# Optimization experiments

Hardware: AMD Instinct MI355X
Metric: run time of the kernel (lower is better)

## Reference

```python
import jax, jax.numpy as jnp
import numpy as np

B, S, D = 32, 4096, 64
EPS_DIV = 1e-8
EPS_LN = 1e-5  # torch LayerNorm default


def setup_inputs() -> dict:
    key = jax.random.key(0)
    k1, k2, k3 = jax.random.split(key, 3)
    C = jax.random.normal(k1, (B, S, D), dtype=jnp.float32)
    V = jax.random.normal(k2, (B, S, D), dtype=jnp.float32)
    W = jax.random.normal(k3, (B, S, D), dtype=jnp.float32)
    time_mod = jnp.ones((1, 1, D), dtype=jnp.float32) * 0.5  # matches init: ones * 0.5
    ln_gamma = jnp.ones((D,), dtype=jnp.float32)
    ln_beta = jnp.zeros((D,), dtype=jnp.float32)
    return {"C": C, "V": V, "W": W, "time_mod": time_mod,
            "ln_gamma": ln_gamma, "ln_beta": ln_beta}


def reference(C, V, W, time_mod, ln_gamma, ln_beta):
    # Precompute elementwise quantities once (fused, no per-step kernels)
    decay = jax.nn.sigmoid(W * time_mod)        # [B,S,D]
    eC = jnp.exp(C)                             # [B,S,D]

    # scan over sequence axis; move S to the front for lax.scan
    xs = (jnp.swapaxes(decay, 0, 1),            # [S,B,D]
          jnp.swapaxes(eC, 0, 1),
          jnp.swapaxes(V, 0, 1))

    a0 = jnp.zeros((C.shape[0], 1), dtype=C.dtype)
    b0 = jnp.zeros((C.shape[0], C.shape[2]), dtype=C.dtype)

    def step(carry, x):
        a, b = carry
        d, ec, v = x                            # each [B,D]
        a = jnp.mean(d, axis=1, keepdims=True) * a + jnp.sum(ec, axis=1, keepdims=True)
        b = d * b + ec * v
        return (a, b), b / (a + EPS_DIV)

    _, ys = jax.lax.scan(step, (a0, b0), xs)    # ys: [S,B,D]
    result = jnp.swapaxes(ys, 0, 1)             # [B,S,D]

    # LayerNorm over last dim
    mu = jnp.mean(result, axis=-1, keepdims=True)
    var = jnp.var(result, axis=-1, keepdims=True)
    normed = (result - mu) * jax.lax.rsqrt(var + EPS_LN)
    return normed * ln_gamma + ln_beta
```

## Files before the change

kernel.cpp:

```cpp
#include <hip/hip_runtime.h>
#include <hip/hip_fp16.h>

constexpr int B = 32, S = 4096, D = 64;
constexpr float EPS_DIV = 1e-8f;
constexpr float EPS_LN  = 1e-5f;

constexpr int NCG = 512;
constexpr int LG  = S / NCG;
constexpr int CPL = NCG / 64;
constexpr int BPB = NCG / 16;

struct alignas(16) H2x4 { __half2 a, b, c, d; };

typedef float        f4v __attribute__((ext_vector_type(4)));
typedef unsigned int u2v __attribute__((ext_vector_type(2)));

__device__ __forceinline__ void nt_store_f4(float4 v, float4* p) {
    f4v t = {v.x, v.y, v.z, v.w};
    __builtin_nontemporal_store(t, (f4v*)p);
}

__device__ __forceinline__ float sigmoid_f(float x) {
    return __builtin_amdgcn_rcpf(1.f + __expf(-x));
}

__global__ __launch_bounds__(256, 4) void k1h(
    const float4* __restrict__ C4, const float4* __restrict__ V4,
    const float4* __restrict__ W4, const float* __restrict__ TM,
    float2* __restrict__ MQstep,
    float*  __restrict__ Mc, float* __restrict__ Qc,
    H2x4*   __restrict__ POt,
    H2x4*   __restrict__ dgev)
{
    __shared__ float sp[64][17];
    __shared__ float so[64][17];

    const int t = threadIdx.x;
    const int g = t >> 4;
    const int r = t & 15;
    const int G = blockIdx.x * 16 + g;
    const int b = G >> 9;
    const int c = G & (NCG - 1);
    const int c0 = (blockIdx.x & (BPB - 1)) * 16;
    const int s0 = c * LG;
    const size_t base = (size_t)(b * S + s0) * 16 + r;
    const float4 tm = reinterpret_cast<const float4*>(TM)[r];

    float psd[LG], pse[LG];
    float4 P = {1.f, 1.f, 1.f, 1.f}, O = {0.f, 0.f, 0.f, 0.f};
#pragma unroll
    for (int i = 0; i < LG; ++i) {
        const size_t idx = base + (size_t)i * 16;
        const float4 w = W4[idx], cc = C4[idx], v = V4[idx];
        float4 dg, ec;
        dg.x = sigmoid_f(w.x * tm.x); dg.y = sigmoid_f(w.y * tm.y);
        dg.z = sigmoid_f(w.z * tm.z); dg.w = sigmoid_f(w.w * tm.w);
        ec.x = __expf(cc.x); ec.y = __expf(cc.y);
        ec.z = __expf(cc.z); ec.w = __expf(cc.w);
        psd[i] = (dg.x + dg.y) + (dg.z + dg.w);
        pse[i] = (ec.x + ec.y) + (ec.z + ec.w);
        H2x4 hq;
        hq.a = __floats2half2_rn(dg.x, ec.x * v.x);
        hq.b = __floats2half2_rn(dg.y, ec.y * v.y);
        hq.c = __floats2half2_rn(dg.z, ec.z * v.z);
        hq.d = __floats2half2_rn(dg.w, ec.w * v.w);
        dgev[idx] = hq;
        const float2 f0 = __half22float2(hq.a);
        const float2 f1 = __half22float2(hq.b);
        const float2 f2 = __half22float2(hq.c);
        const float2 f3 = __half22float2(hq.d);
        P.x *= f0.x; P.y *= f1.x; P.z *= f2.x; P.w *= f3.x;
        O.x = fmaf(f0.x, O.x, f0.y);
        O.y = fmaf(f1.x, O.y, f1.y);
        O.z = fmaf(f2.x, O.z, f2.y);
        O.w = fmaf(f3.x, O.w, f3.y);
    }

#pragma unroll
    for (int m = 1; m < 16; m <<= 1) {
#pragma unroll
        for (int i = 0; i < LG; ++i) {
            psd[i] += __shfl_xor(psd[i], m, 64);
            pse[i] += __shfl_xor(pse[i], m, 64);
        }
    }
    float M = 1.f, Q = 0.f;
#pragma unroll
    for (int i = 0; i < LG; ++i) {
        const float mm = psd[i] * (1.f / 64.f);
        M *= mm;
        Q  = fmaf(mm, Q, pse[i]);
    }
    if (r == 0) {
#pragma unroll
        for (int i = 0; i < LG; ++i)
            MQstep[b * S + s0 + i] = make_float2(psd[i] * (1.f / 64.f), pse[i]);
        Mc[G] = M; Qc[G] = Q;
    }

    sp[4*r+0][g] = P.x; sp[4*r+1][g] = P.y; sp[4*r+2][g] = P.z; sp[4*r+3][g] = P.w;
    so[4*r+0][g] = O.x; so[4*r+1][g] = O.y; so[4*r+2][g] = O.z; so[4*r+3][g] = O.w;
    __syncthreads();
    const int d  = t >> 2;
    const int cq = t & 3;
    H2x4 po;
    po.a = __floats2half2_rn(sp[d][cq*4+0], so[d][cq*4+0]);
    po.b = __floats2half2_rn(sp[d][cq*4+1], so[d][cq*4+1]);
    po.c = __floats2half2_rn(sp[d][cq*4+2], so[d][cq*4+2]);
    po.d = __floats2half2_rn(sp[d][cq*4+3], so[d][cq*4+3]);
    POt[(size_t)(b * D + d) * (NCG / 4) + (c0 >> 2) + cq] = po;
}

__global__ __launch_bounds__(256) void k2(
    const float*  __restrict__ Mc,  const float*  __restrict__ Qc,
    const H2x4*   __restrict__ POt,
    float4* __restrict__ aIn4,
    H2x4*   __restrict__ bInH)
{
    const int wq   = threadIdx.x >> 6;
    const int lane = threadIdx.x & 63;

    if (blockIdx.x < 512) {
        const int W = blockIdx.x * 4 + wq;
        const int b = W >> 6, d = W & 63;
        const size_t row4 = (size_t)(b * D + d) * (NCG / 4);
        const H2x4 A = POt[row4 + lane*2], Bq = POt[row4 + lane*2 + 1];
        float pj[CPL], oj[CPL];
        {
            float2 f;
            f = __half22float2(A.a);  pj[0] = f.x; oj[0] = f.y;
            f = __half22float2(A.b);  pj[1] = f.x; oj[1] = f.y;
            f = __half22float2(A.c);  pj[2] = f.x; oj[2] = f.y;
            f = __half22float2(A.d);  pj[3] = f.x; oj[3] = f.y;
            f = __half22float2(Bq.a); pj[4] = f.x; oj[4] = f.y;
            f = __half22float2(Bq.b); pj[5] = f.x; oj[5] = f.y;
            f = __half22float2(Bq.c); pj[6] = f.x; oj[6] = f.y;
            f = __half22float2(Bq.d); pj[7] = f.x; oj[7] = f.y;
        }
        float p = 1.f, o = 0.f;
#pragma unroll
        for (int j = 0; j < CPL; ++j) { o = fmaf(pj[j], o, oj[j]); p = pj[j] * p; }
#pragma unroll
        for (int s = 1; s < 64; s <<= 1) {
            const float pp = __shfl_up(p, s, 64);
            const float oo = __shfl_up(o, s, 64);
            if (lane >= s) { o = fmaf(p, oo, o); p = p * pp; }
        }
        float oe = __shfl_up(o, 1, 64);
        if (lane == 0) oe = 0.f;
        float bv = oe, ob[CPL];
#pragma unroll
        for (int j = 0; j < CPL; ++j) { ob[j] = bv; bv = fmaf(pj[j], bv, oj[j]); }
        H2x4 w;
        w.a = __floats2half2_rn(ob[0], ob[1]);
        w.b = __floats2half2_rn(ob[2], ob[3]);
        w.c = __floats2half2_rn(ob[4], ob[5]);
        w.d = __floats2half2_rn(ob[6], ob[7]);
        bInH[(size_t)(b * D + d) * (NCG / 8) + lane] = w;
    } else {
        const int v = (blockIdx.x - 512) * 4 + wq;
        if (v >= B) return;
        const float4* Mc4 = reinterpret_cast<const float4*>(Mc) + v * (NCG / 4);
        const float4* Qc4 = reinterpret_cast<const float4*>(Qc) + v * (NCG / 4);
        const float4 mA = Mc4[lane*2], mB = Mc4[lane*2 + 1];
        const float4 qA = Qc4[lane*2], qB = Qc4[lane*2 + 1];
        float mj[CPL] = {mA.x, mA.y, mA.z, mA.w, mB.x, mB.y, mB.z, mB.w};
        float qj[CPL] = {qA.x, qA.y, qA.z, qA.w, qB.x, qB.y, qB.z, qB.w};
        float m = 1.f, q = 0.f;
#pragma unroll
        for (int j = 0; j < CPL; ++j) { q = fmaf(mj[j], q, qj[j]); m = mj[j] * m; }
#pragma unroll
        for (int s = 1; s < 64; s <<= 1) {
            const float mm = __shfl_up(m, s, 64);
            const float qq = __shfl_up(q, s, 64);
            if (lane >= s) { q = fmaf(m, qq, q); m = m * mm; }
        }
        float qe = __shfl_up(q, 1, 64);
        if (lane == 0) qe = 0.f;
        float a = qe, ab[CPL];
#pragma unroll
        for (int j = 0; j < CPL; ++j) { ab[j] = a; a = fmaf(mj[j], a, qj[j]); }
        aIn4[v * (NCG / 4) + lane*2]     = make_float4(ab[0], ab[1], ab[2], ab[3]);
        aIn4[v * (NCG / 4) + lane*2 + 1] = make_float4(ab[4], ab[5], ab[6], ab[7]);
    }
}

__global__ __launch_bounds__(256, 4) void k3h(
    const H2x4* __restrict__ dgev,
    const float* __restrict__ Gam, const float* __restrict__ Bet,
    const float2* __restrict__ MQstep,
    const float* __restrict__ aIn, const __half* __restrict__ bInH,
    float4* __restrict__ out4)
{
    __shared__ float sb[64][17];

    const int t = threadIdx.x;
    const int b  = blockIdx.x >> 5;
    const int c0 = (blockIdx.x & (BPB - 1)) * 16;
    {
        const int d = t >> 2, cq = t & 3;
        const u2v raw = *reinterpret_cast<const u2v*>(
            bInH + (size_t)(b * D + d) * NCG + c0 + cq * 4);
        union { unsigned int u; __half2 h; } c0u, c1u;
        c0u.u = raw.x; c1u.u = raw.y;
        const float2 f0 = __half22float2(c0u.h);
        const float2 f1 = __half22float2(c1u.h);
        sb[d][cq*4+0] = f0.x; sb[d][cq*4+1] = f0.y;
        sb[d][cq*4+2] = f1.x; sb[d][cq*4+3] = f1.y;
    }
    __syncthreads();

    const int g = t >> 4;
    const int r = t & 15;
    const int c = c0 + g;
    const int s0 = c * LG;
    const size_t base = (size_t)(b * S + s0) * 16 + r;
    const float4 g4 = reinterpret_cast<const float4*>(Gam)[r];
    const float4 b4 = reinterpret_cast<const float4*>(Bet)[r];

    float a = aIn[b * NCG + c];
    float4 bv = make_float4(sb[4*r+0][g], sb[4*r+1][g],
                            sb[4*r+2][g], sb[4*r+3][g]);

    float4 yv[LG];
    float psy[LG], psq[LG];
#pragma unroll
    for (int i = 0; i < LG; ++i) {
        const size_t idx = base + (size_t)i * 16;
        const H2x4 hq = dgev[idx];
        const float2 f0 = __half22float2(hq.a);
        const float2 f1 = __half22float2(hq.b);
        const float2 f2 = __half22float2(hq.c);
        const float2 f3 = __half22float2(hq.d);
        const float2 mq = MQstep[b * S + s0 + i];
        a = fmaf(mq.x, a, mq.y);
        bv.x = fmaf(f0.x, bv.x, f0.y);
        bv.y = fmaf(f1.x, bv.y, f1.y);
        bv.z = fmaf(f2.x, bv.z, f2.y);
        bv.w = fmaf(f3.x, bv.w, f3.y);
        const float inva = __builtin_amdgcn_rcpf(a + EPS_DIV);
        float4 y;
        y.x = bv.x * inva; y.y = bv.y * inva;
        y.z = bv.z * inva; y.w = bv.w * inva;
        yv[i] = y;
        psy[i] = (y.x + y.y) + (y.z + y.w);
        psq[i] = fmaf(y.x, y.x, y.y * y.y) + fmaf(y.z, y.z, y.w * y.w);
    }
#pragma unroll
    for (int m = 1; m < 16; m <<= 1) {
#pragma unroll
        for (int i = 0; i < LG; ++i) {
            psy[i] += __shfl_xor(psy[i], m, 64);
            psq[i] += __shfl_xor(psq[i], m, 64);
        }
    }
#pragma unroll
    for (int i = 0; i < LG; ++i) {
        const float4 y = yv[i];
        const float mu  = psy[i] * (1.f / 64.f);
        const float var = fmaf(-mu, mu, psq[i] * (1.f / 64.f));
        const float rs  = __builtin_amdgcn_rsqf(fmaxf(var, 0.f) + EPS_LN);
        float4 o;
        o.x = fmaf((y.x - mu) * rs, g4.x, b4.x);
        o.y = fmaf((y.y - mu) * rs, g4.y, b4.y);
        o.z = fmaf((y.z - mu) * rs, g4.z, b4.z);
        o.w = fmaf((y.w - mu) * rs, g4.w, b4.w);
        nt_store_f4(o, &out4[base + (size_t)i * 16]);
    }
}

__global__ __launch_bounds__(64) void k_naive(
    const float* __restrict__ Cp, const float* __restrict__ Vp,
    const float* __restrict__ Wp, const float* __restrict__ TM,
    const float* __restrict__ Gam, const float* __restrict__ Bet,
    float* __restrict__ out)
{
    const int b = blockIdx.x;
    const int lane = threadIdx.x;
    const float tm = TM[lane], g = Gam[lane], bt = Bet[lane];
    float a = 0.f, bv = 0.f;
    for (int s = 0; s < S; ++s) {
        const size_t idx = ((size_t)b * S + s) * D + lane;
        const float wv = Wp[idx], cv = Cp[idx], vv = Vp[idx];
        const float dg = sigmoid_f(wv * tm);
        const float ec = __expf(cv);
        float sd = dg, se = ec;
#pragma unroll
        for (int m = 1; m < 64; m <<= 1) {
            sd += __shfl_xor(sd, m, 64);
            se += __shfl_xor(se, m, 64);
        }
        a  = fmaf(sd * (1.f / 64.f), a, se);
        bv = fmaf(dg, bv, ec * vv);
        const float y = bv * __builtin_amdgcn_rcpf(a + EPS_DIV);
        float sy = y, sq = y * y;
#pragma unroll
        for (int m = 1; m < 64; m <<= 1) {
            sy += __shfl_xor(sy, m, 64);
            sq += __shfl_xor(sq, m, 64);
        }
        const float mu  = sy * (1.f / 64.f);
        const float var = fmaf(-mu, mu, sq * (1.f / 64.f));
        const float rs  = __builtin_amdgcn_rsqf(fmaxf(var, 0.f) + EPS_LN);
        out[idx] = fmaf((y - mu) * rs, g, bt);
    }
}

extern "C" void kernel_launch(void* const* d_in, const int* in_sizes, int n_in,
                              void* d_out, int out_size, void* d_ws, size_t ws_size,
                              hipStream_t stream) {
    const float* Cp  = (const float*)d_in[0];
    const float* Vp  = (const float*)d_in[1];
    const float* Wp  = (const float*)d_in[2];
    const float* TM  = (const float*)d_in[3];
    const float* Gam = (const float*)d_in[4];
    const float* Bet = (const float*)d_in[5];
    float* out = (float*)d_out;
    float* wsf = (float*)d_ws;

    const size_t f_mq   = (size_t)B * S * 2;
    const size_t f_scG  = (size_t)B * NCG;
    const size_t f_vecG = (size_t)B * NCG * D;
    const size_t f_po   = f_vecG;
    const size_t f_binh = f_vecG / 2;
    const size_t f_dgev = (size_t)B * S * D;
    const size_t f_base = f_mq + 2 * f_scG + f_po + f_scG + f_binh;
    const size_t needH  = (f_base + f_dgev) * sizeof(float);

    if (ws_size >= needH) {
        float2* MQstep = (float2*)wsf;
        float*  Mc   = wsf + f_mq;
        float*  Qc   = Mc + f_scG;
        float*  POf  = Qc + f_scG;
        float*  aIn  = POf + f_po;
        float*  bInf = aIn + f_scG;
        H2x4*   dgev = (H2x4*)(wsf + f_base);
        H2x4*   POt  = (H2x4*)POf;
        H2x4*   bInH = (H2x4*)bInf;

        const dim3 blk(256);
        const dim3 grd(B * NCG / 16);

        k1h<<<grd, blk, 0, stream>>>((const float4*)Cp, (const float4*)Vp,
                                     (const float4*)Wp, TM, MQstep, Mc, Qc,
                                     POt, dgev);
        k2<<<dim3(512 + 8), blk, 0, stream>>>(Mc, Qc, POt,
                                              (float4*)aIn, bInH);
        k3h<<<grd, blk, 0, stream>>>(dgev, Gam, Bet, MQstep,
                                     aIn, (const __half*)bInH, (float4*)out);
        return;
    }

    k_naive<<<dim3(B), dim3(64), 0, stream>>>(Cp, Vp, Wp, TM, Gam, Bet, out);
}
```

Measured before the change: 41.36 us.

## Recompute decay and exp terms in final pass instead of storing fp16 intermediate

The first pass no longer writes a packed fp16 (decay, exp(C)*V) buffer. The final pass rereads the original C, V, W inputs and recomputes sigmoid and exp. This removes a 32MB intermediate write and read and the fp16 rounding, at the cost of reading three fp32 inputs again and recomputing transcendentals. Whether it pays off depends on the reread being served from the large last-level cache.

```diff
diff --git a/kernel.cpp b/kernel.cpp
--- a/kernel.cpp
+++ b/kernel.cpp
@@ -29,8 +29,7 @@
     const float4* __restrict__ W4, const float* __restrict__ TM,
     float2* __restrict__ MQstep,
     float*  __restrict__ Mc, float* __restrict__ Qc,
-    H2x4*   __restrict__ POt,
-    H2x4*   __restrict__ dgev)
+    H2x4*   __restrict__ POt)
 {
     __shared__ float sp[64][17];
     __shared__ float so[64][17];
@@ -59,21 +58,11 @@
         ec.z = __expf(cc.z); ec.w = __expf(cc.w);
         psd[i] = (dg.x + dg.y) + (dg.z + dg.w);
         pse[i] = (ec.x + ec.y) + (ec.z + ec.w);
-        H2x4 hq;
-        hq.a = __floats2half2_rn(dg.x, ec.x * v.x);
-        hq.b = __floats2half2_rn(dg.y, ec.y * v.y);
-        hq.c = __floats2half2_rn(dg.z, ec.z * v.z);
-        hq.d = __floats2half2_rn(dg.w, ec.w * v.w);
-        dgev[idx] = hq;
-        const float2 f0 = __half22float2(hq.a);
-        const float2 f1 = __half22float2(hq.b);
-        const float2 f2 = __half22float2(hq.c);
-        const float2 f3 = __half22float2(hq.d);
-        P.x *= f0.x; P.y *= f1.x; P.z *= f2.x; P.w *= f3.x;
-        O.x = fmaf(f0.x, O.x, f0.y);
-        O.y = fmaf(f1.x, O.y, f1.y);
-        O.z = fmaf(f2.x, O.z, f2.y);
-        O.w = fmaf(f3.x, O.w, f3.y);
+        P.x *= dg.x; P.y *= dg.y; P.z *= dg.z; P.w *= dg.w;
+        O.x = fmaf(dg.x, O.x, ec.x * v.x);
+        O.y = fmaf(dg.y, O.y, ec.y * v.y);
+        O.z = fmaf(dg.z, O.z, ec.z * v.z);
+        O.w = fmaf(dg.w, O.w, ec.w * v.w);
     }
 
 #pragma unroll
@@ -185,8 +174,9 @@
     }
 }
 
-__global__ __launch_bounds__(256, 4) void k3h(
-    const H2x4* __restrict__ dgev,
+__global__ __launch_bounds__(256, 4) void k3r(
+    const float4* __restrict__ C4, const float4* __restrict__ V4,
+    const float4* __restrict__ W4, const float* __restrict__ TM,
     const float* __restrict__ Gam, const float* __restrict__ Bet,
     const float2* __restrict__ MQstep,
     const float* __restrict__ aIn, const __half* __restrict__ bInH,
@@ -215,6 +205,7 @@
     const int c = c0 + g;
     const int s0 = c * LG;
     const size_t base = (size_t)(b * S + s0) * 16 + r;
+    const float4 tm = reinterpret_cast<const float4*>(TM)[r];
     const float4 g4 = reinterpret_cast<const float4*>(Gam)[r];
     const float4 b4 = reinterpret_cast<const float4*>(Bet)[r];
 
@@ -227,17 +218,18 @@
 #pragma unroll
     for (int i = 0; i < LG; ++i) {
         const size_t idx = base + (size_t)i * 16;
-        const H2x4 hq = dgev[idx];
-        const float2 f0 = __half22float2(hq.a);
-        const float2 f1 = __half22float2(hq.b);
-        const float2 f2 = __half22float2(hq.c);
-        const float2 f3 = __half22float2(hq.d);
+        const float4 w = W4[idx], cc = C4[idx], v = V4[idx];
+        float4 dg, ec;
+        dg.x = sigmoid_f(w.x * tm.x); dg.y = sigmoid_f(w.y * tm.y);
+        dg.z = sigmoid_f(w.z * tm.z); dg.w = sigmoid_f(w.w * tm.w);
+        ec.x = __expf(cc.x); ec.y = __expf(cc.y);
+        ec.z = __expf(cc.z); ec.w = __expf(cc.w);
         const float2 mq = MQstep[b * S + s0 + i];
         a = fmaf(mq.x, a, mq.y);
-        bv.x = fmaf(f0.x, bv.x, f0.y);
-        bv.y = fmaf(f1.x, bv.y, f1.y);
-        bv.z = fmaf(f2.x, bv.z, f2.y);
-        bv.w = fmaf(f3.x, bv.w, f3.y);
+        bv.x = fmaf(dg.x, bv.x, ec.x * v.x);
+        bv.y = fmaf(dg.y, bv.y, ec.y * v.y);
+        bv.z = fmaf(dg.z, bv.z, ec.z * v.z);
+        bv.w = fmaf(dg.w, bv.w, ec.w * v.w);
         const float inva = __builtin_amdgcn_rcpf(a + EPS_DIV);
         float4 y;
         y.x = bv.x * inva; y.y = bv.y * inva;
@@ -323,9 +315,7 @@
     const size_t f_vecG = (size_t)B * NCG * D;
     const size_t f_po   = f_vecG;
     const size_t f_binh = f_vecG / 2;
-    const size_t f_dgev = (size_t)B * S * D;
-    const size_t f_base = f_mq + 2 * f_scG + f_po + f_scG + f_binh;
-    const size_t needH  = (f_base + f_dgev) * sizeof(float);
+    const size_t needH  = (f_mq + 3 * f_scG + f_po + f_binh) * sizeof(float);
 
     if (ws_size >= needH) {
         float2* MQstep = (float2*)wsf;
@@ -334,7 +324,6 @@
         float*  POf  = Qc + f_scG;
         float*  aIn  = POf + f_po;
         float*  bInf = aIn + f_scG;
-        H2x4*   dgev = (H2x4*)(wsf + f_base);
         H2x4*   POt  = (H2x4*)POf;
         H2x4*   bInH = (H2x4*)bInf;
 
@@ -342,11 +331,11 @@
         const dim3 grd(B * NCG / 16);
 
         k1h<<<grd, blk, 0, stream>>>((const float4*)Cp, (const float4*)Vp,
-                                     (const float4*)Wp, TM, MQstep, Mc, Qc,
-                                     POt, dgev);
+                                     (const float4*)Wp, TM, MQstep, Mc, Qc, POt);
         k2<<<dim3(512 + 8), blk, 0, stream>>>(Mc, Qc, POt,
                                               (float4*)aIn, bInH);
-        k3h<<<grd, blk, 0, stream>>>(dgev, Gam, Bet, MQstep,
+        k3r<<<grd, blk, 0, stream>>>((const float4*)Cp, (const float4*)Vp,
+                                     (const float4*)Wp, TM, Gam, Bet, MQstep,
                                      aIn, (const __half*)bInH, (float4*)out);
         return;
     }
```

Result: slower. 49.21 us (+19.0%).
